# Kernel optimization log

Hardware: AMD Instinct MI355X
Metric: run time of the kernel (lower is better)

The kernel has to match this reference:

```python
import jax, jax.numpy as jnp
import numpy as np

# Constants fixed from the original (module-level image_encoder attrs in source)
ORIGIN_W, ORIGIN_H = 600, 900   # origin_img_size = (W_orig, H_orig)
RESIZE = 518
PATCH = 14
GRID = RESIZE // PATCH          # 37
M_TOKENS = GRID * GRID          # 1369


def setup_inputs() -> dict:
    key = jax.random.key(0)
    ks = jax.random.split(key, 9)
    B, V, NV, DIM, PF, HID, OUT = 2, 65536, 6, 384, 64, 256, 16
    inp = {
        "patch_tokens": jax.random.normal(ks[0], (B, NV, M_TOKENS, DIM), jnp.float32),
        "voxel_features": jax.random.normal(ks[1], (B, V, PF), jnp.float32),
        "voxel_coords": jax.random.normal(ks[2], (B, V, 3), jnp.float32),
        "K": jax.random.normal(ks[3], (3, 3), jnp.float32),
        "Rt": jax.random.normal(ks[4], (3, 4), jnp.float32),
        "W1": jax.random.normal(ks[5], (PF + DIM, HID), jnp.float32) / np.sqrt(PF + DIM),
        "b1": jnp.zeros((HID,), jnp.float32),
        "W2": jax.random.normal(ks[6], (HID, OUT), jnp.float32) / np.sqrt(HID),
        "b2": jnp.zeros((OUT,), jnp.float32),
    }
    return inp


def _project(voxel_coords, K, Rt):
    # points_h: [B, V, 4]
    ones = jnp.ones(voxel_coords.shape[:-1] + (1,), voxel_coords.dtype)
    points_h = jnp.concatenate([voxel_coords, ones], axis=-1)
    cam = jnp.einsum('ij,bvj->bvi', Rt, points_h)   # [B, V, 3]
    pix = jnp.einsum('ij,bvj->bvi', K, cam)          # [B, V, 3]
    u = pix[..., 0] / (pix[..., 2] + 1e-6)
    v = pix[..., 1] / (pix[..., 2] + 1e-6)
    return u, v


def reference(patch_tokens, voxel_features, voxel_coords, K, Rt, W1, b1, W2, b2):
    # Project points to pixel coords, scale to resized image
    u, v = _project(voxel_coords, K, Rt)
    u = u * (RESIZE / ORIGIN_W)
    v = v * (RESIZE / ORIGIN_H)
    # Patch indices (truncate toward zero like torch .long()), clamp to grid
    px = jnp.clip((u / PATCH).astype(jnp.int32), 0, GRID - 1)   # [B, V]
    py = jnp.clip((v / PATCH).astype(jnp.int32), 0, GRID - 1)
    flat_idx = px * GRID + py                                    # [B, V]
    # Indices are identical across views in the source, so mean-over-views of
    # per-view gathers == gather from view-mean tokens (same math, no [B,V,views,dim] blowup)
    mean_tokens = patch_tokens.mean(axis=1)                      # [B, M, dim]
    fused_img_feat = jnp.take_along_axis(mean_tokens, flat_idx[..., None], axis=1)  # [B, V, dim]
    fused = jnp.concatenate([voxel_features, fused_img_feat], axis=-1)
    h = jax.nn.relu(fused @ W1 + b1)
    return h @ W2 + b2
```

## Files before the change

kernel.cpp:

```cpp
#include <hip/hip_runtime.h>
#include <cstdint>
#include <cstddef>

#define BATCH 2
#define NVIEW 6
#define MTOK  1369
#define DIM   384
#define VOXPB 65536
#define PFEAT 64
#define HID   256
#define OUTD  16
#define GRIDN 37

typedef float  f32x4  __attribute__((ext_vector_type(4)));
typedef short  bf16x8 __attribute__((ext_vector_type(8)));
typedef _Float16 f16x4 __attribute__((ext_vector_type(4)));

#define OFF_MEAN 0
#define SZ_MEAN  (BATCH*MTOK*DIM*2)
#define OFF_T    (OFF_MEAN + SZ_MEAN)
#define SZ_T     (BATCH*MTOK*HID*2)
#define OFF_W1B  (OFF_T + SZ_T)
#define SZ_W1B   (DIM*HID*2)
#define OFF_W1A  (OFF_W1B + SZ_W1B)
#define SZ_W1A   (PFEAT*HID*2)
#define OFF_W2T  (OFF_W1A + SZ_W1A)
#define SZ_W2T   (HID*OUTD*2)

__device__ __forceinline__ unsigned short f2bf(float x) {
    unsigned u = __float_as_uint(x);
    unsigned r = (u + 0x7FFFu + ((u >> 16) & 1u)) >> 16;
    return (unsigned short)r;
}

#define MEAN_PAIRS (BATCH*MTOK*DIM/2)
#define MEAN_BLKS  ((MEAN_PAIRS + 255)/256)
#define W1B_BLKS   384
#define W1A_BLKS   64
#define W2T_BLKS   16

__global__ __launch_bounds__(256) void prep_kernel(
    const float* __restrict__ patch, const float* __restrict__ W1,
    const float* __restrict__ W2, unsigned short* __restrict__ ws16)
{
    int blk = blockIdx.x;
    if (blk < MEAN_BLKS) {
        int e = blk*256 + threadIdx.x;
        if (e < MEAN_PAIRS) {
            int row = e / (DIM/2);
            int d2  = e - row*(DIM/2);
            int b = row / MTOK, m = row - b*MTOK;
            const float* p = patch + (((size_t)(b*NVIEW))*MTOK + m)*DIM + d2*2;
            float s0 = 0.f, s1 = 0.f;
            #pragma unroll
            for (int nv = 0; nv < NVIEW; nv++) {
                const float2 v = *(const float2*)(p + (size_t)nv*MTOK*DIM);
                s0 += v.x; s1 += v.y;
            }
            s0 *= (1.0f/6.0f); s1 *= (1.0f/6.0f);
            unsigned short* dst = ws16 + (OFF_MEAN/2) + (size_t)row*DIM + d2*2;
            dst[0] = f2bf(s0); dst[1] = f2bf(s1);
        }
        return;
    }
    blk -= MEAN_BLKS;
    if (blk < W1B_BLKS) {
        int e = blk*256 + threadIdx.x;
        int j = e & 7, lane = (e >> 3) & 63, nt = (e >> 9) & 15, kc = e >> 13;
        int k = kc*32 + (lane >> 4)*8 + j;
        int n = nt*16 + (lane & 15);
        ws16[OFF_W1B/2 + e] = f2bf(W1[(PFEAT + k)*HID + n]);
        return;
    }
    blk -= W1B_BLKS;
    if (blk < W1A_BLKS) {
        int e = blk*256 + threadIdx.x;
        int j = e & 7, lane = (e >> 3) & 63, nt = (e >> 9) & 15, kc = e >> 13;
        int k = kc*32 + (lane >> 4)*8 + j;
        int n = nt*16 + (lane & 15);
        ws16[OFF_W1A/2 + e] = f2bf(W1[k*HID + n]);
        return;
    }
    blk -= W1A_BLKS;
    {
        int e = blk*256 + threadIdx.x;
        int j = e & 3, lane = (e >> 2) & 63, nt = e >> 8;
        int k = nt*16 + (lane >> 4)*4 + j;
        _Float16 v = (_Float16)W2[k*OUTD + (lane & 15)];
        ws16[OFF_W2T/2 + e] = __builtin_bit_cast(unsigned short, v);
    }
}

#define T_ROWS (BATCH*MTOK)
#define T_BLKS ((T_ROWS + 63)/64)
#define APAD   392

__global__ __launch_bounds__(256) void t_gemm_kernel(
    const unsigned short* __restrict__ ws16r, const float* __restrict__ b1,
    unsigned short* __restrict__ ws16)
{
    __shared__ unsigned short Abuf[64*APAD];
    const int tid = threadIdx.x;
    const int tileBase = blockIdx.x*64;

    const uint4* msrc = (const uint4*)(ws16r + OFF_MEAN/2);
    uint4* sA = (uint4*)Abuf;
    for (int i = tid; i < 64*48; i += 256) {
        int row = i / 48, c = i - row*48;
        int gr = tileBase + row;
        uint4 v = make_uint4(0,0,0,0);
        if (gr < T_ROWS) v = msrc[(size_t)gr*48 + c];
        sA[row*(APAD/8) + c] = v;
    }
    __syncthreads();

    const int lane = tid & 63, wv = tid >> 6;
    const int q = lane >> 4, l = lane & 15;
    const uint4* bfr = (const uint4*)(ws16r + OFF_W1B/2);

    f32x4 acc[4][4];
    #pragma unroll
    for (int a = 0; a < 4; a++)
        #pragma unroll
        for (int m = 0; m < 4; m++) acc[a][m] = (f32x4){0.f,0.f,0.f,0.f};

    for (int kc = 0; kc < 12; kc++) {
        bf16x8 bfrag[4];
        #pragma unroll
        for (int ntl = 0; ntl < 4; ntl++) {
            int nt = wv*4 + ntl;
            bfrag[ntl] = __builtin_bit_cast(bf16x8, bfr[(kc*16 + nt)*64 + lane]);
        }
        #pragma unroll
        for (int mt = 0; mt < 4; mt++) {
            const bf16x8 af = *(const bf16x8*)(Abuf + (mt*16 + l)*APAD + kc*32 + q*8);
            #pragma unroll
            for (int ntl = 0; ntl < 4; ntl++)
                acc[ntl][mt] = __builtin_amdgcn_mfma_f32_16x16x32_bf16(
                                   af, bfrag[ntl], acc[ntl][mt], 0, 0, 0);
        }
    }

    unsigned short* T = ws16 + OFF_T/2;
    float bbv[4];
    #pragma unroll
    for (int ntl = 0; ntl < 4; ntl++) bbv[ntl] = b1[(wv*4 + ntl)*16 + l];
    #pragma unroll
    for (int mt = 0; mt < 4; mt++)
        #pragma unroll
        for (int r = 0; r < 4; r++) {
            int row = tileBase + mt*16 + q*4 + r;
            if (row < T_ROWS) {
                ushort4 pk;
                pk.x = f2bf(acc[0][mt][r] + bbv[0]);
                pk.y = f2bf(acc[1][mt][r] + bbv[1]);
                pk.z = f2bf(acc[2][mt][r] + bbv[2]);
                pk.w = f2bf(acc[3][mt][r] + bbv[3]);
                *(ushort4*)(T + (size_t)row*HID + l*16 + wv*4) = pk;
            }
        }
}

__device__ __forceinline__ int proj_idx(float x, float y, float z,
                                        const float* __restrict__ Km,
                                        const float* __restrict__ Rt)
{
    float c0 = __fadd_rn(__fadd_rn(__fadd_rn(__fmul_rn(Rt[0],x), __fmul_rn(Rt[1],y)), __fmul_rn(Rt[2],z)), Rt[3]);
    float c1 = __fadd_rn(__fadd_rn(__fadd_rn(__fmul_rn(Rt[4],x), __fmul_rn(Rt[5],y)), __fmul_rn(Rt[6],z)), Rt[7]);
    float c2 = __fadd_rn(__fadd_rn(__fadd_rn(__fmul_rn(Rt[8],x), __fmul_rn(Rt[9],y)), __fmul_rn(Rt[10],z)), Rt[11]);
    float p0 = __fadd_rn(__fadd_rn(__fmul_rn(Km[0],c0), __fmul_rn(Km[1],c1)), __fmul_rn(Km[2],c2));
    float p1 = __fadd_rn(__fadd_rn(__fmul_rn(Km[3],c0), __fmul_rn(Km[4],c1)), __fmul_rn(Km[5],c2));
    float p2 = __fadd_rn(__fadd_rn(__fmul_rn(Km[6],c0), __fmul_rn(Km[7],c1)), __fmul_rn(Km[8],c2));
    float zz = __fadd_rn(p2, 1e-6f);
    float u  = __fmul_rn(__fdiv_rn(p0, zz), 518.0f/600.0f);
    float v  = __fmul_rn(__fdiv_rn(p1, zz), 518.0f/900.0f);
    float fu = __fdiv_rn(u, 14.0f);
    float fv = __fdiv_rn(v, 14.0f);
    int px = (__builtin_fabsf(fu) < 2147483648.0f) ? (int)fu : (int)0x80000000;
    int py = (__builtin_fabsf(fv) < 2147483648.0f) ? (int)fv : (int)0x80000000;
    px = min(max(px, 0), GRIDN-1);
    py = min(max(py, 0), GRIDN-1);
    return px*GRIDN + py;
}

__global__ __launch_bounds__(256, 4) void main_kernel(
    const float* __restrict__ vf, const float* __restrict__ coords,
    const float* __restrict__ Km, const float* __restrict__ Rt,
    const unsigned short* __restrict__ ws16, const float* __restrict__ b2,
    float* __restrict__ out)
{
    __shared__ uint4 w1aS[2048];
    __shared__ int   idxS[128];

    const int tid = threadIdx.x;
    const uint4* w1aG = (const uint4*)(ws16 + OFF_W1A/2);
    #pragma unroll
    for (int i = 0; i < 8; i++) w1aS[i*256 + tid] = w1aG[i*256 + tid];

    if (tid < 128) {
        int vox = blockIdx.x*128 + tid;
        const float* cp = coords + (size_t)vox*3;
        idxS[tid] = proj_idx(cp[0], cp[1], cp[2], Km, Rt);
    }
    __syncthreads();

    const int lane = tid & 63, wv = tid >> 6;
    const int q = lane >> 4, l = lane & 15;
    const int voxBase = blockIdx.x*128 + wv*32;
    const int b = blockIdx.x >> 9;

    bf16x8 a1[2][2];
    #pragma unroll
    for (int mt = 0; mt < 2; mt++) {
        const float* vp = vf + (size_t)(voxBase + mt*16 + l)*PFEAT;
        #pragma unroll
        for (int kc = 0; kc < 2; kc++) {
            const float* pp = vp + kc*32 + q*8;
            f32x4 v0 = *(const f32x4*)pp;
            f32x4 v1 = *(const f32x4*)(pp + 4);
            bf16x8 f;
            f[0]=f2bf(v0[0]); f[1]=f2bf(v0[1]); f[2]=f2bf(v0[2]); f[3]=f2bf(v0[3]);
            f[4]=f2bf(v1[0]); f[5]=f2bf(v1[1]); f[6]=f2bf(v1[2]); f[7]=f2bf(v1[3]);
            a1[mt][kc] = f;
        }
    }

    const unsigned short* T = ws16 + OFF_T/2;
    uint4 tra[2][4][2];
    #pragma unroll
    for (int mt = 0; mt < 2; mt++)
        #pragma unroll
        for (int r = 0; r < 4; r++) {
            int row = b*MTOK + idxS[wv*32 + mt*16 + q*4 + r];
            const uint4* tp = (const uint4*)(T + (size_t)row*HID + l*16);
            tra[mt][r][0] = tp[0];
            tra[mt][r][1] = tp[1];
        }

    const unsigned short* w2tG = ws16 + OFF_W2T/2;

    f16x4 ident;
    #pragma unroll
    for (int j = 0; j < 4; j++)
        ident[j] = (q*4 + j == l) ? (_Float16)1.0f : (_Float16)0.0f;

    const f32x4 zero4 = {0.f,0.f,0.f,0.f};
    f32x4 acc2[2] = {zero4, zero4};

    #pragma unroll
    for (int nt = 0; nt < 16; nt++) {
        bf16x8 wf0 = __builtin_bit_cast(bf16x8, w1aS[nt*64 + lane]);
        bf16x8 wf1 = __builtin_bit_cast(bf16x8, w1aS[(16 + nt)*64 + lane]);
        f16x4 w2t = *(const f16x4*)(w2tG + (nt*64 + lane)*4);
        #pragma unroll
        for (int mt = 0; mt < 2; mt++) {
            f32x4 d1 = __builtin_amdgcn_mfma_f32_16x16x32_bf16(a1[mt][0], wf0, zero4, 0, 0, 0);
            d1       = __builtin_amdgcn_mfma_f32_16x16x32_bf16(a1[mt][1], wf1, d1,    0, 0, 0);
            f16x4 aT;
            #pragma unroll
            for (int r = 0; r < 4; r++) {
                unsigned dw = ((const unsigned*)&tra[mt][r])[nt >> 1];
                float tval = (nt & 1) ? __uint_as_float(dw & 0xFFFF0000u)
                                      : __uint_as_float(dw << 16);
                float v = fmaxf(d1[r] + tval, 0.0f);
                aT[r] = (_Float16)v;
            }
            f32x4 ht = __builtin_amdgcn_mfma_f32_16x16x16f16(aT, ident, zero4, 0, 0, 0);
            f16x4 hb;
            hb[0]=(_Float16)ht[0]; hb[1]=(_Float16)ht[1];
            hb[2]=(_Float16)ht[2]; hb[3]=(_Float16)ht[3];
            acc2[mt] = __builtin_amdgcn_mfma_f32_16x16x16f16(w2t, hb, acc2[mt], 0, 0, 0);
        }
    }

    f32x4 bb = *(const f32x4*)(b2 + q*4);
    #pragma unroll
    for (int mt = 0; mt < 2; mt++) {
        f32x4 o = acc2[mt] + bb;
        *(f32x4*)(out + (size_t)(voxBase + mt*16 + l)*OUTD + q*4) = o;
    }
}

extern "C" void kernel_launch(void* const* d_in, const int* in_sizes, int n_in,
                              void* d_out, int out_size, void* d_ws, size_t ws_size,
                              hipStream_t stream)
{
    const float* patch  = (const float*)d_in[0];
    const float* vfeat  = (const float*)d_in[1];
    const float* coords = (const float*)d_in[2];
    const float* Km     = (const float*)d_in[3];
    const float* Rt     = (const float*)d_in[4];
    const float* W1     = (const float*)d_in[5];
    const float* b1     = (const float*)d_in[6];
    const float* W2     = (const float*)d_in[7];
    const float* b2     = (const float*)d_in[8];
    float* out          = (float*)d_out;
    unsigned short* ws16 = (unsigned short*)d_ws;

    const int prepBlocks = MEAN_BLKS + W1B_BLKS + W1A_BLKS + W2T_BLKS;
    prep_kernel<<<prepBlocks, 256, 0, stream>>>(patch, W1, W2, ws16);
    t_gemm_kernel<<<T_BLKS, 256, 0, stream>>>(ws16, b1, ws16);
    main_kernel<<<(BATCH*VOXPB)/128, 256, 0, stream>>>(vfeat, coords, Km, Rt,
                                                       ws16, b2, out);
}
```

Baseline: 127.9 us.

## Fuse view-mean into token GEMM and shrink tiles for both GEMM kernels

The view-averaging of patch tokens moves out of the prep kernel and into the token GEMM's shared-memory load, so the bf16 mean buffer no longer makes a round trip through global memory. The token GEMM tile drops from 64 to 16 rows, giving many more blocks, and the main voxel kernel handles 64 voxels per block instead of 128, doubling its grid. The intent is less memory traffic and better occupancy. The cost is that each W1 fragment is re-read from global once per 16-row tile, and each main block repeats the shared W1a staging for half as many voxels.

```diff
diff --git a/kernel.cpp b/kernel.cpp
--- a/kernel.cpp
+++ b/kernel.cpp
@@ -16,9 +16,7 @@
 typedef short  bf16x8 __attribute__((ext_vector_type(8)));
 typedef _Float16 f16x4 __attribute__((ext_vector_type(4)));
 
-#define OFF_MEAN 0
-#define SZ_MEAN  (BATCH*MTOK*DIM*2)
-#define OFF_T    (OFF_MEAN + SZ_MEAN)
+#define OFF_T    0
 #define SZ_T     (BATCH*MTOK*HID*2)
 #define OFF_W1B  (OFF_T + SZ_T)
 #define SZ_W1B   (DIM*HID*2)
@@ -33,37 +31,15 @@
     return (unsigned short)r;
 }
 
-#define MEAN_PAIRS (BATCH*MTOK*DIM/2)
-#define MEAN_BLKS  ((MEAN_PAIRS + 255)/256)
 #define W1B_BLKS   384
 #define W1A_BLKS   64
 #define W2T_BLKS   16
 
 __global__ __launch_bounds__(256) void prep_kernel(
-    const float* __restrict__ patch, const float* __restrict__ W1,
-    const float* __restrict__ W2, unsigned short* __restrict__ ws16)
+    const float* __restrict__ W1, const float* __restrict__ W2,
+    unsigned short* __restrict__ ws16)
 {
     int blk = blockIdx.x;
-    if (blk < MEAN_BLKS) {
-        int e = blk*256 + threadIdx.x;
-        if (e < MEAN_PAIRS) {
-            int row = e / (DIM/2);
-            int d2  = e - row*(DIM/2);
-            int b = row / MTOK, m = row - b*MTOK;
-            const float* p = patch + (((size_t)(b*NVIEW))*MTOK + m)*DIM + d2*2;
-            float s0 = 0.f, s1 = 0.f;
-            #pragma unroll
-            for (int nv = 0; nv < NVIEW; nv++) {
-                const float2 v = *(const float2*)(p + (size_t)nv*MTOK*DIM);
-                s0 += v.x; s1 += v.y;
-            }
-            s0 *= (1.0f/6.0f); s1 *= (1.0f/6.0f);
-            unsigned short* dst = ws16 + (OFF_MEAN/2) + (size_t)row*DIM + d2*2;
-            dst[0] = f2bf(s0); dst[1] = f2bf(s1);
-        }
-        return;
-    }
-    blk -= MEAN_BLKS;
     if (blk < W1B_BLKS) {
         int e = blk*256 + threadIdx.x;
         int j = e & 7, lane = (e >> 3) & 63, nt = (e >> 9) & 15, kc = e >> 13;
@@ -92,25 +68,36 @@
 }
 
 #define T_ROWS (BATCH*MTOK)
-#define T_BLKS ((T_ROWS + 63)/64)
+#define TM     16
+#define T_BLKS ((T_ROWS + TM - 1)/TM)
 #define APAD   392
 
 __global__ __launch_bounds__(256) void t_gemm_kernel(
-    const unsigned short* __restrict__ ws16r, const float* __restrict__ b1,
-    unsigned short* __restrict__ ws16)
-{
-    __shared__ unsigned short Abuf[64*APAD];
+    const float* __restrict__ patch, const unsigned short* __restrict__ ws16r,
+    const float* __restrict__ b1, unsigned short* __restrict__ ws16)
+{
+    __shared__ unsigned short Abuf[TM*APAD];
     const int tid = threadIdx.x;
-    const int tileBase = blockIdx.x*64;
-
-    const uint4* msrc = (const uint4*)(ws16r + OFF_MEAN/2);
-    uint4* sA = (uint4*)Abuf;
-    for (int i = tid; i < 64*48; i += 256) {
-        int row = i / 48, c = i - row*48;
+    const int tileBase = blockIdx.x*TM;
+
+    #pragma unroll
+    for (int it = 0; it < 6; it++) {
+        int i = it*256 + tid;
+        int row = i / 96, c = i - row*96;
         int gr = tileBase + row;
-        uint4 v = make_uint4(0,0,0,0);
-        if (gr < T_ROWS) v = msrc[(size_t)gr*48 + c];
-        sA[row*(APAD/8) + c] = v;
+        f32x4 s = {0.f,0.f,0.f,0.f};
+        if (gr < T_ROWS) {
+            int b = (gr >= MTOK) ? 1 : 0;
+            int m = gr - b*MTOK;
+            const float* p = patch + (((size_t)(b*NVIEW))*MTOK + m)*DIM + c*4;
+            #pragma unroll
+            for (int nv = 0; nv < NVIEW; nv++)
+                s += *(const f32x4*)(p + (size_t)nv*MTOK*DIM);
+            s *= (1.0f/6.0f);
+        }
+        ushort4 pk;
+        pk.x = f2bf(s[0]); pk.y = f2bf(s[1]); pk.z = f2bf(s[2]); pk.w = f2bf(s[3]);
+        *(ushort4*)(Abuf + row*APAD + c*4) = pk;
     }
     __syncthreads();
 
@@ -118,26 +105,16 @@
     const int q = lane >> 4, l = lane & 15;
     const uint4* bfr = (const uint4*)(ws16r + OFF_W1B/2);
 
-    f32x4 acc[4][4];
-    #pragma unroll
-    for (int a = 0; a < 4; a++)
-        #pragma unroll
-        for (int m = 0; m < 4; m++) acc[a][m] = (f32x4){0.f,0.f,0.f,0.f};
+    f32x4 acc[4];
+    #pragma unroll
+    for (int a = 0; a < 4; a++) acc[a] = (f32x4){0.f,0.f,0.f,0.f};
 
     for (int kc = 0; kc < 12; kc++) {
-        bf16x8 bfrag[4];
+        const bf16x8 af = *(const bf16x8*)(Abuf + l*APAD + kc*32 + q*8);
         #pragma unroll
         for (int ntl = 0; ntl < 4; ntl++) {
-            int nt = wv*4 + ntl;
-            bfrag[ntl] = __builtin_bit_cast(bf16x8, bfr[(kc*16 + nt)*64 + lane]);
-        }
-        #pragma unroll
-        for (int mt = 0; mt < 4; mt++) {
-            const bf16x8 af = *(const bf16x8*)(Abuf + (mt*16 + l)*APAD + kc*32 + q*8);
-            #pragma unroll
-            for (int ntl = 0; ntl < 4; ntl++)
-                acc[ntl][mt] = __builtin_amdgcn_mfma_f32_16x16x32_bf16(
-                                   af, bfrag[ntl], acc[ntl][mt], 0, 0, 0);
+            bf16x8 bfrag = __builtin_bit_cast(bf16x8, bfr[(kc*16 + wv*4 + ntl)*64 + lane]);
+            acc[ntl] = __builtin_amdgcn_mfma_f32_16x16x32_bf16(af, bfrag, acc[ntl], 0, 0, 0);
         }
     }
 
@@ -146,19 +123,17 @@
     #pragma unroll
     for (int ntl = 0; ntl < 4; ntl++) bbv[ntl] = b1[(wv*4 + ntl)*16 + l];
     #pragma unroll
-    for (int mt = 0; mt < 4; mt++)
-        #pragma unroll
-        for (int r = 0; r < 4; r++) {
-            int row = tileBase + mt*16 + q*4 + r;
-            if (row < T_ROWS) {
-                ushort4 pk;
-                pk.x = f2bf(acc[0][mt][r] + bbv[0]);
-                pk.y = f2bf(acc[1][mt][r] + bbv[1]);
-                pk.z = f2bf(acc[2][mt][r] + bbv[2]);
-                pk.w = f2bf(acc[3][mt][r] + bbv[3]);
-                *(ushort4*)(T + (size_t)row*HID + l*16 + wv*4) = pk;
-            }
-        }
+    for (int r = 0; r < 4; r++) {
+        int row = tileBase + q*4 + r;
+        if (row < T_ROWS) {
+            ushort4 pk;
+            pk.x = f2bf(acc[0][r] + bbv[0]);
+            pk.y = f2bf(acc[1][r] + bbv[1]);
+            pk.z = f2bf(acc[2][r] + bbv[2]);
+            pk.w = f2bf(acc[3][r] + bbv[3]);
+            *(ushort4*)(T + (size_t)row*HID + l*16 + wv*4) = pk;
+        }
+    }
 }
 
 __device__ __forceinline__ int proj_idx(float x, float y, float z,
@@ -190,15 +165,15 @@
     float* __restrict__ out)
 {
     __shared__ uint4 w1aS[2048];
-    __shared__ int   idxS[128];
+    __shared__ int   idxS[64];
 
     const int tid = threadIdx.x;
     const uint4* w1aG = (const uint4*)(ws16 + OFF_W1A/2);
     #pragma unroll
     for (int i = 0; i < 8; i++) w1aS[i*256 + tid] = w1aG[i*256 + tid];
 
-    if (tid < 128) {
-        int vox = blockIdx.x*128 + tid;
+    if (tid < 64) {
+        int vox = blockIdx.x*64 + tid;
         const float* cp = coords + (size_t)vox*3;
         idxS[tid] = proj_idx(cp[0], cp[1], cp[2], Km, Rt);
     }
@@ -206,13 +181,12 @@
 
     const int lane = tid & 63, wv = tid >> 6;
     const int q = lane >> 4, l = lane & 15;
-    const int voxBase = blockIdx.x*128 + wv*32;
-    const int b = blockIdx.x >> 9;
-
-    bf16x8 a1[2][2];
-    #pragma unroll
-    for (int mt = 0; mt < 2; mt++) {
-        const float* vp = vf + (size_t)(voxBase + mt*16 + l)*PFEAT;
+    const int voxG = blockIdx.x*64 + wv*16;
+    const int b = blockIdx.x >> 10;
+
+    bf16x8 a1[2];
+    {
+        const float* vp = vf + (size_t)(voxG + l)*PFEAT;
         #pragma unroll
         for (int kc = 0; kc < 2; kc++) {
             const float* pp = vp + kc*32 + q*8;
@@ -221,21 +195,19 @@
             bf16x8 f;
             f[0]=f2bf(v0[0]); f[1]=f2bf(v0[1]); f[2]=f2bf(v0[2]); f[3]=f2bf(v0[3]);
             f[4]=f2bf(v1[0]); f[5]=f2bf(v1[1]); f[6]=f2bf(v1[2]); f[7]=f2bf(v1[3]);
-            a1[mt][kc] = f;
+            a1[kc] = f;
         }
     }
 
     const unsigned short* T = ws16 + OFF_T/2;
-    uint4 tra[2][4][2];
-    #pragma unroll
-    for (int mt = 0; mt < 2; mt++)
-        #pragma unroll
-        for (int r = 0; r < 4; r++) {
-            int row = b*MTOK + idxS[wv*32 + mt*16 + q*4 + r];
-            const uint4* tp = (const uint4*)(T + (size_t)row*HID + l*16);
-            tra[mt][r][0] = tp[0];
-            tra[mt][r][1] = tp[1];
-        }
+    uint4 tra[4][2];
+    #pragma unroll
+    for (int r = 0; r < 4; r++) {
+        int row = b*MTOK + idxS[wv*16 + q*4 + r];
+        const uint4* tp = (const uint4*)(T + (size_t)row*HID + l*16);
+        tra[r][0] = tp[0];
+        tra[r][1] = tp[1];
+    }
 
     const unsigned short* w2tG = ws16 + OFF_W2T/2;
 
@@ -245,40 +217,34 @@
         ident[j] = (q*4 + j == l) ? (_Float16)1.0f : (_Float16)0.0f;
 
     const f32x4 zero4 = {0.f,0.f,0.f,0.f};
-    f32x4 acc2[2] = {zero4, zero4};
+    f32x4 acc2 = zero4;
 
     #pragma unroll
     for (int nt = 0; nt < 16; nt++) {
         bf16x8 wf0 = __builtin_bit_cast(bf16x8, w1aS[nt*64 + lane]);
         bf16x8 wf1 = __builtin_bit_cast(bf16x8, w1aS[(16 + nt)*64 + lane]);
         f16x4 w2t = *(const f16x4*)(w2tG + (nt*64 + lane)*4);
+        f32x4 d1 = __builtin_amdgcn_mfma_f32_16x16x32_bf16(a1[0], wf0, zero4, 0, 0, 0);
+        d1       = __builtin_amdgcn_mfma_f32_16x16x32_bf16(a1[1], wf1, d1,    0, 0, 0);
+        f16x4 aT;
         #pragma unroll
-        for (int mt = 0; mt < 2; mt++) {
-            f32x4 d1 = __builtin_amdgcn_mfma_f32_16x16x32_bf16(a1[mt][0], wf0, zero4, 0, 0, 0);
-            d1       = __builtin_amdgcn_mfma_f32_16x16x32_bf16(a1[mt][1], wf1, d1,    0, 0, 0);
-            f16x4 aT;
-            #pragma unroll
-            for (int r = 0; r < 4; r++) {
-                unsigned dw = ((const unsigned*)&tra[mt][r])[nt >> 1];
-                float tval = (nt & 1) ? __uint_as_float(dw & 0xFFFF0000u)
-                                      : __uint_as_float(dw << 16);
-                float v = fmaxf(d1[r] + tval, 0.0f);
-                aT[r] = (_Float16)v;
-            }
-            f32x4 ht = __builtin_amdgcn_mfma_f32_16x16x16f16(aT, ident, zero4, 0, 0, 0);
-            f16x4 hb;
-            hb[0]=(_Float16)ht[0]; hb[1]=(_Float16)ht[1];
-            hb[2]=(_Float16)ht[2]; hb[3]=(_Float16)ht[3];
-            acc2[mt] = __builtin_amdgcn_mfma_f32_16x16x16f16(w2t, hb, acc2[mt], 0, 0, 0);
-        }
+        for (int r = 0; r < 4; r++) {
+            unsigned dw = ((const unsigned*)&tra[r])[nt >> 1];
+            float tval = (nt & 1) ? __uint_as_float(dw & 0xFFFF0000u)
+                                  : __uint_as_float(dw << 16);
+            float v = fmaxf(d1[r] + tval, 0.0f);
+            aT[r] = (_Float16)v;
+        }
+        f32x4 ht = __builtin_amdgcn_mfma_f32_16x16x16f16(aT, ident, zero4, 0, 0, 0);
+        f16x4 hb;
+        hb[0]=(_Float16)ht[0]; hb[1]=(_Float16)ht[1];
+        hb[2]=(_Float16)ht[2]; hb[3]=(_Float16)ht[3];
+        acc2 = __builtin_amdgcn_mfma_f32_16x16x16f16(w2t, hb, acc2, 0, 0, 0);
     }
 
     f32x4 bb = *(const f32x4*)(b2 + q*4);
-    #pragma unroll
-    for (int mt = 0; mt < 2; mt++) {
-        f32x4 o = acc2[mt] + bb;
-        *(f32x4*)(out + (size_t)(voxBase + mt*16 + l)*OUTD + q*4) = o;
-    }
+    f32x4 o = acc2 + bb;
+    *(f32x4*)(out + (size_t)(voxG + l)*OUTD + q*4) = o;
 }
 
 extern "C" void kernel_launch(void* const* d_in, const int* in_sizes, int n_in,
@@ -297,9 +263,9 @@
     float* out          = (float*)d_out;
     unsigned short* ws16 = (unsigned short*)d_ws;
 
-    const int prepBlocks = MEAN_BLKS + W1B_BLKS + W1A_BLKS + W2T_BLKS;
-    prep_kernel<<<prepBlocks, 256, 0, stream>>>(patch, W1, W2, ws16);
-    t_gemm_kernel<<<T_BLKS, 256, 0, stream>>>(ws16, b1, ws16);
-    main_kernel<<<(BATCH*VOXPB)/128, 256, 0, stream>>>(vfeat, coords, Km, Rt,
-                                                       ws16, b2, out);
-}
+    const int prepBlocks = W1B_BLKS + W1A_BLKS + W2T_BLKS;
+    prep_kernel<<<prepBlocks, 256, 0, stream>>>(W1, W2, ws16);
+    t_gemm_kernel<<<T_BLKS, 256, 0, stream>>>(patch, ws16, b1, ws16);
+    main_kernel<<<(BATCH*VOXPB)/64, 256, 0, stream>>>(vfeat, coords, Km, Rt,
+                                                      ws16, b2, out);
+}
```

After: 121.1 us. 5.3% less time.
